# Kernel tuning notes

Measured on AMD Instinct MI355X. Metric: run time of the kernel, lower is better.

The kernel has to match this reference:

```python
import jax, jax.numpy as jnp
import numpy as np

S, B, H = 512, 256, 500


def setup_inputs() -> dict:
    key = jax.random.key(0)
    k1, k2, k3, k4, k5 = jax.random.split(key, 5)
    return {
        "hidden": jax.random.normal(k1, (1, B, H), dtype=jnp.float32),
        "encoder_output": jax.random.normal(k2, (S, B, H), dtype=jnp.float32),
        "W_attn": jax.random.normal(k3, (H, 2 * H), dtype=jnp.float32) * 0.02,
        "b_attn": jax.random.normal(k4, (H,), dtype=jnp.float32) * 0.02,
        "v": jax.random.normal(k5, (H,), dtype=jnp.float32),
    }


def reference(hidden, encoder_output, W_attn, b_attn, v):
    # hidden: [1, B, H] -> broadcast to [S, B, H]; concat -> [S, B, 2H]
    s, b, h = encoder_output.shape
    h_exp = jnp.broadcast_to(hidden, (s, b, h))
    cat = jnp.concatenate([h_exp, encoder_output], axis=2)  # [S, B, 2H]
    # Linear(2H -> H) with torch convention W: [out, in], then tanh
    energy = jnp.tanh(jnp.einsum("sbi,hi->sbh", cat, W_attn) + b_attn)  # [S, B, H]
    scores = jnp.einsum("sbh,h->sb", energy, v)  # [S, B]
    attn = jax.nn.softmax(scores.T, axis=1)  # [B, S]
    return attn[:, None, :]  # [B, 1, S]
```

## Files before the change

### kernel.cpp

```cpp
#include <hip/hip_runtime.h>
#include <hip/hip_fp16.h>

#define S_DIM 512
#define B_DIM 256
#define H_DIM 500
#define HP    512
#define M_DIM (S_DIM * B_DIM)

typedef _Float16 half8_t __attribute__((ext_vector_type(8)));
typedef float    f32x4  __attribute__((ext_vector_type(4)));

#define WS_W2R 0
#define WS_AT  (512 * 1024)
#define WS_VP  (1024 * 1024)
#define WS_SC  (1024 * 1024 + 4096)

__global__ void prep_w2_v(const float* __restrict__ W, const float* __restrict__ v,
                          _Float16* __restrict__ W2r, float* __restrict__ vp) {
    int idx = blockIdx.x * blockDim.x + threadIdx.x;
#pragma unroll
    for (int r = 0; r < 2; ++r) {
        int e = idx + r * 131072;
        int n = e >> 9, k = e & 511;
        float val = (n < H_DIM && k < H_DIM) ? W[n * 1000 + 500 + k] : 0.0f;
        int dst = ((n >> 4) * 64 + (k >> 3)) * 128 + (n & 15) * 8 + (k & 7);
        W2r[dst] = (_Float16)val;
    }
    if (idx < HP) vp[idx] = (idx < H_DIM) ? v[idx] : 0.0f;
}

__global__ void prep_A(const float* __restrict__ hidden, const float* __restrict__ W,
                       const float* __restrict__ b_attn, float* __restrict__ At) {
    int b = blockIdx.x;
    int t = threadIdx.x;
    __shared__ float hs[HP];
    hs[t] = (t < H_DIM) ? hidden[b * H_DIM + t] : 0.0f;
    __syncthreads();
    float acc = 0.0f;
    if (t < H_DIM) {
        acc = b_attn[t];
        const float4* wr = (const float4*)(W + t * 1000);
        const float4* hr = (const float4*)hs;
#pragma unroll 5
        for (int i = 0; i < 125; ++i) {
            float4 w4 = wr[i], h4 = hr[i];
            acc += w4.x * h4.x + w4.y * h4.y + w4.z * h4.z + w4.w * h4.w;
        }
    }
    At[t * B_DIM + b] = acc;
}

__launch_bounds__(256, 2)
__global__ void fused_attn_gemm(const float* __restrict__ enc,
                                const _Float16* __restrict__ W2r,
                                const float* __restrict__ At,
                                const float* __restrict__ vp,
                                float* __restrict__ sct) {
    __shared__ _Float16 As[2][128][32];
    __shared__ float    red[2][128];

    const int tid  = threadIdx.x;
    const int lane = tid & 63;
    const int wid  = tid >> 6;
    const int wm   = wid >> 1;
    const int wn   = wid & 1;
    const int l15  = lane & 15;
    const int lq   = lane >> 4;

    const int mblk = blockIdx.x;
    const int m0   = mblk * 128;
    const int bloc = (mblk & 1) * 128;
    const int s_idx = mblk >> 1;

    const int r0  = tid >> 2;
    const int r1  = r0 + 64;
    const int cst = tid & 3;
    const float* gA0 = enc + (size_t)(m0 + r0) * H_DIM + cst * 8;
    const float* gA1 = enc + (size_t)(m0 + r1) * H_DIM + cst * 8;
    const int ca0 = (cst ^ ((r0 >> 1) & 3)) * 8;
    const int ca1 = (cst ^ ((r1 >> 1) & 3)) * 8;

    const int rch = (lq ^ ((l15 >> 1) & 3)) * 8;

    const _Float16* gB = W2r + wn * 32768 + lq * 128 + l15 * 8;

    f32x4 a00, a01, a10, a11;
    auto ldA = [&](int kk) {
        if (kk != 480) {
            a00 = *(const f32x4*)(gA0 + kk); a01 = *(const f32x4*)(gA0 + kk + 4);
            a10 = *(const f32x4*)(gA1 + kk); a11 = *(const f32x4*)(gA1 + kk + 4);
        } else {
#pragma unroll
            for (int u = 0; u < 4; ++u) {
                int k = kk + cst * 8 + u;
                a00[u] = (k < H_DIM) ? gA0[kk + u] : 0.0f;
                a10[u] = (k < H_DIM) ? gA1[kk + u] : 0.0f;
                int k2 = k + 4;
                a01[u] = (k2 < H_DIM) ? gA0[kk + 4 + u] : 0.0f;
                a11[u] = (k2 < H_DIM) ? gA1[kk + 4 + u] : 0.0f;
            }
        }
    };
    auto wrA = [&](int buf) {
        half8_t h0, h1;
#pragma unroll
        for (int u = 0; u < 4; ++u) {
            h0[u] = (_Float16)a00[u]; h0[u + 4] = (_Float16)a01[u];
            h1[u] = (_Float16)a10[u]; h1[u + 4] = (_Float16)a11[u];
        }
        *(half8_t*)&As[buf][r0][ca0] = h0;
        *(half8_t*)&As[buf][r1][ca1] = h1;
    };

    float pj[4][4];
#pragma unroll
    for (int mf = 0; mf < 4; ++mf)
#pragma unroll
        for (int j = 0; j < 4; ++j) pj[mf][j] = 0.0f;

    for (int nc = 0; nc < 4; ++nc) {
        f32x4 acc[4][4];
#pragma unroll
        for (int a = 0; a < 4; ++a)
#pragma unroll
            for (int b = 0; b < 4; ++b) acc[a][b] = 0;

        ldA(0);
        wrA(0);

#pragma unroll
        for (int ks = 0; ks < 16; ++ks) {
            __syncthreads();
            if (ks < 15) ldA((ks + 1) * 32);

            half8_t bfc[4];
#pragma unroll
            for (int nf = 0; nf < 4; ++nf)
                bfc[nf] = *(const half8_t*)(gB + nc * 65536 + nf * 8192 + ks * 512);

            half8_t af[4];
#pragma unroll
            for (int mf = 0; mf < 4; ++mf)
                af[mf] = *(const half8_t*)&As[ks & 1][wm * 64 + mf * 16 + l15][rch];

#pragma unroll
            for (int mf = 0; mf < 4; ++mf)
#pragma unroll
                for (int nf = 0; nf < 4; ++nf)
                    acc[mf][nf] = __builtin_amdgcn_mfma_f32_16x16x32_f16(af[mf], bfc[nf], acc[mf][nf], 0, 0, 0);

            if (ks < 15) wrA((ks & 1) ^ 1);
        }

        float vpv[4];
#pragma unroll
        for (int nf = 0; nf < 4; ++nf) vpv[nf] = vp[nc * 128 + wn * 64 + nf * 16 + l15];

#pragma unroll
        for (int mf = 0; mf < 4; ++mf) {
#pragma unroll
            for (int nf = 0; nf < 4; ++nf) {
                int h = nc * 128 + wn * 64 + nf * 16 + l15;
                f32x4 av = *(const f32x4*)(At + h * B_DIM + bloc + wm * 64 + mf * 16 + lq * 4);
#pragma unroll
                for (int j = 0; j < 4; ++j) {
                    float x  = acc[mf][nf][j] + av[j];
                    float xc = fminf(fmaxf(x, -9.0f), 9.0f);
                    float e  = __expf(2.0f * xc);
                    float th = (e - 1.0f) / (e + 1.0f);
                    pj[mf][j] += vpv[nf] * th;
                }
            }
        }
    }

#pragma unroll
    for (int mf = 0; mf < 4; ++mf)
#pragma unroll
        for (int j = 0; j < 4; ++j) {
            float s = pj[mf][j];
            s += __shfl_xor(s, 1); s += __shfl_xor(s, 2);
            s += __shfl_xor(s, 4); s += __shfl_xor(s, 8);
            if (l15 == 0) red[wn][wm * 64 + mf * 16 + lq * 4 + j] = s;
        }
    __syncthreads();
    if (tid < 128) {
        float p = red[0][tid] + red[1][tid];
        sct[(size_t)(bloc + tid) * S_DIM + s_idx] = p;
    }
}

__global__ void softmax_rows(const float* __restrict__ sct, float* __restrict__ out) {
    int b = blockIdx.x;
    int t = threadIdx.x;
    int lane = t & 63, w = t >> 6;
    float v = sct[(size_t)b * S_DIM + t];
    float m = v;
#pragma unroll
    for (int off = 1; off < 64; off <<= 1) m = fmaxf(m, __shfl_xor(m, off));
    __shared__ float sm[8], ss[8];
    if (lane == 0) sm[w] = m;
    __syncthreads();
    m = sm[0];
#pragma unroll
    for (int i = 1; i < 8; ++i) m = fmaxf(m, sm[i]);
    float e = __expf(v - m);
    float s = e;
#pragma unroll
    for (int off = 1; off < 64; off <<= 1) s += __shfl_xor(s, off);
    if (lane == 0) ss[w] = s;
    __syncthreads();
    s = ss[0];
#pragma unroll
    for (int i = 1; i < 8; ++i) s += ss[i];
    out[(size_t)b * S_DIM + t] = e / s;
}

extern "C" void kernel_launch(void* const* d_in, const int* in_sizes, int n_in,
                              void* d_out, int out_size, void* d_ws, size_t ws_size,
                              hipStream_t stream) {
    const float* hidden = (const float*)d_in[0];
    const float* enc    = (const float*)d_in[1];
    const float* W      = (const float*)d_in[2];
    const float* b_attn = (const float*)d_in[3];
    const float* v      = (const float*)d_in[4];
    float* out = (float*)d_out;

    char* ws = (char*)d_ws;
    _Float16* W2r = (_Float16*)(ws + WS_W2R);
    float*    At  = (float*)(ws + WS_AT);
    float*    vp  = (float*)(ws + WS_VP);
    float*    sct = (float*)(ws + WS_SC);

    prep_w2_v<<<512, 256, 0, stream>>>(W, v, W2r, vp);
    prep_A<<<256, 512, 0, stream>>>(hidden, W, b_attn, At);
    fused_attn_gemm<<<1024, 256, 0, stream>>>(enc, W2r, At, vp, sct);
    softmax_rows<<<256, 512, 0, stream>>>(sct, out);
}
```

Before: 226.0 us.

## Stage full-N weight tile in LDS via async global_load_lds and shrink M tile

The fused GEMM kernel now computes all 512 output columns per block in one pass over K, with 64 rows per block and 512 threads. The weight matrix is pre-laid out as a swizzled LDS image and streamed into double-buffered shared memory with direct global-to-LDS loads. Previously each warp read B fragments straight from global memory and looped over four N chunks, reloading the encoder tile each time. This removes the fourfold re-read and conversion of the encoder input, but costs a much larger LDS footprint (about 72KB per block) and may limit occupancy despite the launch bounds.

```diff
diff --git a/kernel.cpp b/kernel.cpp
--- a/kernel.cpp
+++ b/kernel.cpp
@@ -10,21 +10,28 @@
 typedef _Float16 half8_t __attribute__((ext_vector_type(8)));
 typedef float    f32x4  __attribute__((ext_vector_type(4)));
 
-#define WS_W2R 0
+#define WS_W2I 0
 #define WS_AT  (512 * 1024)
 #define WS_VP  (1024 * 1024)
 #define WS_SC  (1024 * 1024 + 4096)
 
+__device__ __forceinline__ void gld_lds16(const void* g, void* l) {
+    __builtin_amdgcn_global_load_lds(
+        (const __attribute__((address_space(1))) unsigned int*)g,
+        (__attribute__((address_space(3))) unsigned int*)l, 16, 0, 0);
+}
+
 __global__ void prep_w2_v(const float* __restrict__ W, const float* __restrict__ v,
-                          _Float16* __restrict__ W2r, float* __restrict__ vp) {
+                          _Float16* __restrict__ W2img, float* __restrict__ vp) {
     int idx = blockIdx.x * blockDim.x + threadIdx.x;
 #pragma unroll
     for (int r = 0; r < 2; ++r) {
         int e = idx + r * 131072;
         int n = e >> 9, k = e & 511;
         float val = (n < H_DIM && k < H_DIM) ? W[n * 1000 + 500 + k] : 0.0f;
-        int dst = ((n >> 4) * 64 + (k >> 3)) * 128 + (n & 15) * 8 + (k & 7);
-        W2r[dst] = (_Float16)val;
+        int ks = k >> 5, ce = (k >> 3) & 3, u = k & 7;
+        int cL = ce ^ ((n >> 1) & 3);
+        W2img[((ks * 512 + n) * 4 + cL) * 8 + u] = (_Float16)val;
     }
     if (idx < HP) vp[idx] = (idx < H_DIM) ? v[idx] : 0.0f;
 }
@@ -50,142 +57,132 @@
     At[t * B_DIM + b] = acc;
 }
 
-__launch_bounds__(256, 2)
+__launch_bounds__(512, 4)
 __global__ void fused_attn_gemm(const float* __restrict__ enc,
-                                const _Float16* __restrict__ W2r,
+                                const _Float16* __restrict__ W2img,
                                 const float* __restrict__ At,
                                 const float* __restrict__ vp,
                                 float* __restrict__ sct) {
-    __shared__ _Float16 As[2][128][32];
-    __shared__ float    red[2][128];
+    __shared__ _Float16 As[2][64][32];
+    __shared__ _Float16 Bs[2][512][32];
+    __shared__ float    red[4][64];
 
     const int tid  = threadIdx.x;
     const int lane = tid & 63;
     const int wid  = tid >> 6;
-    const int wm   = wid >> 1;
-    const int wn   = wid & 1;
+    const int wm   = wid >> 2;
+    const int wn   = wid & 3;
     const int l15  = lane & 15;
     const int lq   = lane >> 4;
 
-    const int mblk = blockIdx.x;
-    const int m0   = mblk * 128;
-    const int bloc = (mblk & 1) * 128;
-    const int s_idx = mblk >> 1;
-
-    const int r0  = tid >> 2;
-    const int r1  = r0 + 64;
-    const int cst = tid & 3;
-    const float* gA0 = enc + (size_t)(m0 + r0) * H_DIM + cst * 8;
-    const float* gA1 = enc + (size_t)(m0 + r1) * H_DIM + cst * 8;
-    const int ca0 = (cst ^ ((r0 >> 1) & 3)) * 8;
-    const int ca1 = (cst ^ ((r1 >> 1) & 3)) * 8;
+    const int mblk  = blockIdx.x;
+    const int m0    = mblk * 64;
+    const int s_idx = mblk >> 2;
+    const int bloc  = (mblk & 3) * 64;
+
+    const bool aw = (tid < 256);
+    const int  r  = tid >> 2;
+    const int  c  = tid & 3;
+    const float* gA = enc + (size_t)(m0 + (r & 63)) * H_DIM + c * 8;
+    const int  ca = (c ^ ((r >> 1) & 3)) * 8;
 
     const int rch = (lq ^ ((l15 >> 1) & 3)) * 8;
 
-    const _Float16* gB = W2r + wn * 32768 + lq * 128 + l15 * 8;
-
-    f32x4 a00, a01, a10, a11;
+    f32x4 a0, a1;
     auto ldA = [&](int kk) {
         if (kk != 480) {
-            a00 = *(const f32x4*)(gA0 + kk); a01 = *(const f32x4*)(gA0 + kk + 4);
-            a10 = *(const f32x4*)(gA1 + kk); a11 = *(const f32x4*)(gA1 + kk + 4);
+            a0 = *(const f32x4*)(gA + kk);
+            a1 = *(const f32x4*)(gA + kk + 4);
         } else {
 #pragma unroll
             for (int u = 0; u < 4; ++u) {
-                int k = kk + cst * 8 + u;
-                a00[u] = (k < H_DIM) ? gA0[kk + u] : 0.0f;
-                a10[u] = (k < H_DIM) ? gA1[kk + u] : 0.0f;
-                int k2 = k + 4;
-                a01[u] = (k2 < H_DIM) ? gA0[kk + 4 + u] : 0.0f;
-                a11[u] = (k2 < H_DIM) ? gA1[kk + 4 + u] : 0.0f;
+                int k = kk + c * 8 + u;
+                a0[u] = (k < H_DIM) ? gA[kk + u] : 0.0f;
+                a1[u] = (k + 4 < H_DIM) ? gA[kk + 4 + u] : 0.0f;
             }
         }
     };
     auto wrA = [&](int buf) {
-        half8_t h0, h1;
-#pragma unroll
-        for (int u = 0; u < 4; ++u) {
-            h0[u] = (_Float16)a00[u]; h0[u + 4] = (_Float16)a01[u];
-            h1[u] = (_Float16)a10[u]; h1[u + 4] = (_Float16)a11[u];
-        }
-        *(half8_t*)&As[buf][r0][ca0] = h0;
-        *(half8_t*)&As[buf][r1][ca1] = h1;
+        half8_t h;
+#pragma unroll
+        for (int u = 0; u < 4; ++u) { h[u] = (_Float16)a0[u]; h[u + 4] = (_Float16)a1[u]; }
+        *(half8_t*)&As[buf][r & 63][ca] = h;
     };
-
-    float pj[4][4];
-#pragma unroll
-    for (int mf = 0; mf < 4; ++mf)
+    auto stB = [&](int buf, int ksrc) {
+        const _Float16* gbase = W2img + (size_t)ksrc * 16384;
+#pragma unroll
+        for (int i = 0; i < 4; ++i) {
+            int slotb = wid * 256 + i * 64;
+            gld_lds16(gbase + (size_t)(slotb + lane) * 8, (_Float16*)&Bs[buf][0][0] + slotb * 8);
+        }
+    };
+
+    f32x4 acc[2][8];
+#pragma unroll
+    for (int a = 0; a < 2; ++a)
+#pragma unroll
+        for (int b = 0; b < 8; ++b) acc[a][b] = 0;
+
+    stB(0, 0);
+    if (aw) { ldA(0); wrA(0); }
+
+    for (int ks = 0; ks < 16; ++ks) {
+        const int cur = ks & 1;
+        __syncthreads();
+        if (ks < 15) {
+            stB(cur ^ 1, ks + 1);
+            if (aw) ldA((ks + 1) * 32);
+        }
+        half8_t af0 = *(const half8_t*)&As[cur][wm * 32 + l15][rch];
+        half8_t af1 = *(const half8_t*)&As[cur][wm * 32 + 16 + l15][rch];
+#pragma unroll
+        for (int nf = 0; nf < 8; ++nf) {
+            half8_t b = *(const half8_t*)&Bs[cur][wn * 128 + nf * 16 + l15][rch];
+            acc[0][nf] = __builtin_amdgcn_mfma_f32_16x16x32_f16(af0, b, acc[0][nf], 0, 0, 0);
+            acc[1][nf] = __builtin_amdgcn_mfma_f32_16x16x32_f16(af1, b, acc[1][nf], 0, 0, 0);
+        }
+        if (ks < 15 && aw) wrA(cur ^ 1);
+    }
+
+    float vpv[8];
+#pragma unroll
+    for (int nf = 0; nf < 8; ++nf) vpv[nf] = vp[wn * 128 + nf * 16 + l15];
+
+    float pj[2][4];
+#pragma unroll
+    for (int mf = 0; mf < 2; ++mf)
 #pragma unroll
         for (int j = 0; j < 4; ++j) pj[mf][j] = 0.0f;
 
-    for (int nc = 0; nc < 4; ++nc) {
-        f32x4 acc[4][4];
-#pragma unroll
-        for (int a = 0; a < 4; ++a)
-#pragma unroll
-            for (int b = 0; b < 4; ++b) acc[a][b] = 0;
-
-        ldA(0);
-        wrA(0);
-
-#pragma unroll
-        for (int ks = 0; ks < 16; ++ks) {
-            __syncthreads();
-            if (ks < 15) ldA((ks + 1) * 32);
-
-            half8_t bfc[4];
-#pragma unroll
-            for (int nf = 0; nf < 4; ++nf)
-                bfc[nf] = *(const half8_t*)(gB + nc * 65536 + nf * 8192 + ks * 512);
-
-            half8_t af[4];
-#pragma unroll
-            for (int mf = 0; mf < 4; ++mf)
-                af[mf] = *(const half8_t*)&As[ks & 1][wm * 64 + mf * 16 + l15][rch];
-
-#pragma unroll
-            for (int mf = 0; mf < 4; ++mf)
-#pragma unroll
-                for (int nf = 0; nf < 4; ++nf)
-                    acc[mf][nf] = __builtin_amdgcn_mfma_f32_16x16x32_f16(af[mf], bfc[nf], acc[mf][nf], 0, 0, 0);
-
-            if (ks < 15) wrA((ks & 1) ^ 1);
-        }
-
-        float vpv[4];
-#pragma unroll
-        for (int nf = 0; nf < 4; ++nf) vpv[nf] = vp[nc * 128 + wn * 64 + nf * 16 + l15];
-
-#pragma unroll
-        for (int mf = 0; mf < 4; ++mf) {
-#pragma unroll
-            for (int nf = 0; nf < 4; ++nf) {
-                int h = nc * 128 + wn * 64 + nf * 16 + l15;
-                f32x4 av = *(const f32x4*)(At + h * B_DIM + bloc + wm * 64 + mf * 16 + lq * 4);
-#pragma unroll
-                for (int j = 0; j < 4; ++j) {
-                    float x  = acc[mf][nf][j] + av[j];
-                    float xc = fminf(fmaxf(x, -9.0f), 9.0f);
-                    float e  = __expf(2.0f * xc);
-                    float th = (e - 1.0f) / (e + 1.0f);
-                    pj[mf][j] += vpv[nf] * th;
-                }
+#pragma unroll
+    for (int mf = 0; mf < 2; ++mf) {
+#pragma unroll
+        for (int nf = 0; nf < 8; ++nf) {
+            int h = wn * 128 + nf * 16 + l15;
+            f32x4 av = *(const f32x4*)(At + h * B_DIM + bloc + wm * 32 + mf * 16 + lq * 4);
+#pragma unroll
+            for (int j = 0; j < 4; ++j) {
+                float x  = acc[mf][nf][j] + av[j];
+                float xc = fminf(fmaxf(x, -9.0f), 9.0f);
+                float e  = __expf(2.0f * xc);
+                float th = (e - 1.0f) / (e + 1.0f);
+                pj[mf][j] += vpv[nf] * th;
             }
         }
     }
 
 #pragma unroll
-    for (int mf = 0; mf < 4; ++mf)
+    for (int mf = 0; mf < 2; ++mf)
 #pragma unroll
         for (int j = 0; j < 4; ++j) {
             float s = pj[mf][j];
             s += __shfl_xor(s, 1); s += __shfl_xor(s, 2);
             s += __shfl_xor(s, 4); s += __shfl_xor(s, 8);
-            if (l15 == 0) red[wn][wm * 64 + mf * 16 + lq * 4 + j] = s;
-        }
-    __syncthreads();
-    if (tid < 128) {
-        float p = red[0][tid] + red[1][tid];
+            if (l15 == 0) red[wn][wm * 32 + mf * 16 + lq * 4 + j] = s;
+        }
+    __syncthreads();
+    if (tid < 64) {
+        float p = red[0][tid] + red[1][tid] + red[2][tid] + red[3][tid];
         sct[(size_t)(bloc + tid) * S_DIM + s_idx] = p;
     }
 }
@@ -227,13 +224,13 @@
     float* out = (float*)d_out;
 
     char* ws = (char*)d_ws;
-    _Float16* W2r = (_Float16*)(ws + WS_W2R);
+    _Float16* W2i = (_Float16*)(ws + WS_W2I);
     float*    At  = (float*)(ws + WS_AT);
     float*    vp  = (float*)(ws + WS_VP);
     float*    sct = (float*)(ws + WS_SC);
 
-    prep_w2_v<<<512, 256, 0, stream>>>(W, v, W2r, vp);
+    prep_w2_v<<<512, 256, 0, stream>>>(W, v, W2i, vp);
     prep_A<<<256, 512, 0, stream>>>(hidden, W, b_attn, At);
-    fused_attn_gemm<<<1024, 256, 0, stream>>>(enc, W2r, At, vp, sct);
+    fused_attn_gemm<<<2048, 512, 0, stream>>>(enc, W2i, At, vp, sct);
     softmax_rows<<<256, 512, 0, stream>>>(sct, out);
 }
```

New measurement: 187.2 us. 1.21x faster.

## Widen GEMM block to cover full N so encoder tile is loaded once

Applied to the files above, without the earlier changes.

The fused GEMM block grows to 512 threads in a 2x4 wave grid, with each wave computing 128 output columns in a single pass. This replaces four sequential N chunks that each re-streamed and re-converted the fp32 encoder rows. It also adds a two-slice-ahead register prefetch with a hand-written LDS barrier, and simplifies the K-tail loads. The cost is 128 accumulator floats per thread, which raises register pressure and may reduce occupancy.

```diff
diff --git a/kernel.cpp b/kernel.cpp
--- a/kernel.cpp
+++ b/kernel.cpp
@@ -8,6 +8,7 @@
 #define M_DIM (S_DIM * B_DIM)
 
 typedef _Float16 half8_t __attribute__((ext_vector_type(8)));
+typedef _Float16 half4_t __attribute__((ext_vector_type(4)));
 typedef float    f32x4  __attribute__((ext_vector_type(4)));
 
 #define WS_W2R 0
@@ -50,142 +51,145 @@
     At[t * B_DIM + b] = acc;
 }
 
-__launch_bounds__(256, 2)
+__launch_bounds__(512, 2)
 __global__ void fused_attn_gemm(const float* __restrict__ enc,
                                 const _Float16* __restrict__ W2r,
                                 const float* __restrict__ At,
                                 const float* __restrict__ vp,
                                 float* __restrict__ sct) {
     __shared__ _Float16 As[2][128][32];
-    __shared__ float    red[2][128];
+    __shared__ float    red[4][128];
 
     const int tid  = threadIdx.x;
     const int lane = tid & 63;
     const int wid  = tid >> 6;
-    const int wm   = wid >> 1;
-    const int wn   = wid & 1;
+    const int wm   = wid >> 2;
+    const int wn   = wid & 3;
     const int l15  = lane & 15;
     const int lq   = lane >> 4;
 
-    const int mblk = blockIdx.x;
-    const int m0   = mblk * 128;
-    const int bloc = (mblk & 1) * 128;
+    const int mblk  = blockIdx.x;
+    const int m0    = mblk * 128;
     const int s_idx = mblk >> 1;
-
-    const int r0  = tid >> 2;
-    const int r1  = r0 + 64;
-    const int cst = tid & 3;
-    const float* gA0 = enc + (size_t)(m0 + r0) * H_DIM + cst * 8;
-    const float* gA1 = enc + (size_t)(m0 + r1) * H_DIM + cst * 8;
-    const int ca0 = (cst ^ ((r0 >> 1) & 3)) * 8;
-    const int ca1 = (cst ^ ((r1 >> 1) & 3)) * 8;
-
+    const int bloc  = (mblk & 1) * 128;
+
+    const int r0 = tid >> 3;
+    const int r1 = r0 + 64;
+    const int j  = tid & 7;
+    const float* gA0 = enc + (size_t)(m0 + r0) * H_DIM + j * 4;
+    const float* gA1 = enc + (size_t)(m0 + r1) * H_DIM + j * 4;
+    const int jt = (j < 4) ? j : 4;
+    const float* gT0 = enc + (size_t)(m0 + r0) * H_DIM + 480 + jt * 4;
+    const float* gT1 = enc + (size_t)(m0 + r1) * H_DIM + 480 + jt * 4;
+    const bool jz = (j >= 5);
+    const int aoff = ((j >> 1) ^ ((r0 >> 1) & 3)) * 8 + (j & 1) * 4;
     const int rch = (lq ^ ((l15 >> 1) & 3)) * 8;
 
-    const _Float16* gB = W2r + wn * 32768 + lq * 128 + l15 * 8;
-
-    f32x4 a00, a01, a10, a11;
-    auto ldA = [&](int kk) {
-        if (kk != 480) {
-            a00 = *(const f32x4*)(gA0 + kk); a01 = *(const f32x4*)(gA0 + kk + 4);
-            a10 = *(const f32x4*)(gA1 + kk); a11 = *(const f32x4*)(gA1 + kk + 4);
-        } else {
-#pragma unroll
-            for (int u = 0; u < 4; ++u) {
-                int k = kk + cst * 8 + u;
-                a00[u] = (k < H_DIM) ? gA0[kk + u] : 0.0f;
-                a10[u] = (k < H_DIM) ? gA1[kk + u] : 0.0f;
-                int k2 = k + 4;
-                a01[u] = (k2 < H_DIM) ? gA0[kk + 4 + u] : 0.0f;
-                a11[u] = (k2 < H_DIM) ? gA1[kk + 4 + u] : 0.0f;
+    const _Float16* gB = W2r + wn * 65536 + lq * 128 + l15 * 8;
+
+    f32x4 acc[4][8];
+#pragma unroll
+    for (int a = 0; a < 4; ++a)
+#pragma unroll
+        for (int b = 0; b < 8; ++b) acc[a][b] = 0;
+
+    f32x4 pe0, pe1, po0, po1;
+
+    auto ldA = [&](int slice, f32x4& d0, f32x4& d1) {
+        if (slice == 15) { d0 = *(const f32x4*)gT0; d1 = *(const f32x4*)gT1; }
+        else { d0 = *(const f32x4*)(gA0 + slice * 32); d1 = *(const f32x4*)(gA1 + slice * 32); }
+    };
+    auto wrA = [&](int buf, f32x4 d0, f32x4 d1, bool tail) {
+        half4_t h0, h1;
+#pragma unroll
+        for (int u = 0; u < 4; ++u) {
+            h0[u] = (tail && jz) ? (_Float16)0.0f : (_Float16)d0[u];
+            h1[u] = (tail && jz) ? (_Float16)0.0f : (_Float16)d1[u];
+        }
+        *(half4_t*)&As[buf][r0][aoff] = h0;
+        *(half4_t*)&As[buf][r1][aoff] = h1;
+    };
+
+#define BAR() do {                                             \
+        asm volatile("s_waitcnt lgkmcnt(0)" ::: "memory");     \
+        __builtin_amdgcn_sched_barrier(0);                     \
+        __builtin_amdgcn_s_barrier();                          \
+        __builtin_amdgcn_sched_barrier(0);                     \
+    } while (0)
+
+#define KBODY(KS, CUR, WR0, WR1, LD0, LD1)                                     \
+    {                                                                          \
+        half8_t bq[8];                                                         \
+        _Pragma("unroll")                                                      \
+        for (int nf = 0; nf < 8; ++nf)                                         \
+            bq[nf] = *(const half8_t*)(gB + nf * 8192 + (KS) * 512);           \
+        if ((KS) + 2 < 16) ldA((KS) + 2, LD0, LD1);                            \
+        half8_t af[4];                                                         \
+        _Pragma("unroll")                                                      \
+        for (int mf = 0; mf < 4; ++mf)                                         \
+            af[mf] = *(const half8_t*)&As[CUR][wm * 64 + mf * 16 + l15][rch];  \
+        _Pragma("unroll")                                                      \
+        for (int nf = 0; nf < 8; ++nf) {                                       \
+            _Pragma("unroll")                                                  \
+            for (int mf = 0; mf < 4; ++mf)                                     \
+                acc[mf][nf] = __builtin_amdgcn_mfma_f32_16x16x32_f16(          \
+                    af[mf], bq[nf], acc[mf][nf], 0, 0, 0);                     \
+        }                                                                      \
+        if ((KS) + 1 < 16) wrA((CUR) ^ 1, WR0, WR1, (KS) + 1 == 15);           \
+        BAR();                                                                 \
+    }
+
+    ldA(0, pe0, pe1);
+    wrA(0, pe0, pe1, false);
+    ldA(1, po0, po1);
+    BAR();
+
+    for (int kk = 0; kk < 16; kk += 2) {
+        KBODY(kk,     0, po0, po1, pe0, pe1)
+        KBODY(kk + 1, 1, pe0, pe1, po0, po1)
+    }
+#undef KBODY
+#undef BAR
+
+    float vpv[8];
+#pragma unroll
+    for (int nf = 0; nf < 8; ++nf) vpv[nf] = vp[wn * 128 + nf * 16 + l15];
+
+    float pj[4][4];
+#pragma unroll
+    for (int mf = 0; mf < 4; ++mf)
+#pragma unroll
+        for (int jj = 0; jj < 4; ++jj) pj[mf][jj] = 0.0f;
+
+#pragma unroll
+    for (int mf = 0; mf < 4; ++mf) {
+#pragma unroll
+        for (int nf = 0; nf < 8; ++nf) {
+            int h = wn * 128 + nf * 16 + l15;
+            f32x4 av = *(const f32x4*)(At + h * B_DIM + bloc + wm * 64 + mf * 16 + lq * 4);
+#pragma unroll
+            for (int jj = 0; jj < 4; ++jj) {
+                float x  = acc[mf][nf][jj] + av[jj];
+                float xc = fminf(fmaxf(x, -9.0f), 9.0f);
+                float e  = __expf(2.0f * xc);
+                float th = (e - 1.0f) / (e + 1.0f);
+                pj[mf][jj] += vpv[nf] * th;
             }
         }
-    };
-    auto wrA = [&](int buf) {
-        half8_t h0, h1;
-#pragma unroll
-        for (int u = 0; u < 4; ++u) {
-            h0[u] = (_Float16)a00[u]; h0[u + 4] = (_Float16)a01[u];
-            h1[u] = (_Float16)a10[u]; h1[u + 4] = (_Float16)a11[u];
-        }
-        *(half8_t*)&As[buf][r0][ca0] = h0;
-        *(half8_t*)&As[buf][r1][ca1] = h1;
-    };
-
-    float pj[4][4];
+    }
+
 #pragma unroll
     for (int mf = 0; mf < 4; ++mf)
 #pragma unroll
-        for (int j = 0; j < 4; ++j) pj[mf][j] = 0.0f;
-
-    for (int nc = 0; nc < 4; ++nc) {
-        f32x4 acc[4][4];
-#pragma unroll
-        for (int a = 0; a < 4; ++a)
-#pragma unroll
-            for (int b = 0; b < 4; ++b) acc[a][b] = 0;
-
-        ldA(0);
-        wrA(0);
-
-#pragma unroll
-        for (int ks = 0; ks < 16; ++ks) {
-            __syncthreads();
-            if (ks < 15) ldA((ks + 1) * 32);
-
-            half8_t bfc[4];
-#pragma unroll
-            for (int nf = 0; nf < 4; ++nf)
-                bfc[nf] = *(const half8_t*)(gB + nc * 65536 + nf * 8192 + ks * 512);
-
-            half8_t af[4];
-#pragma unroll
-            for (int mf = 0; mf < 4; ++mf)
-                af[mf] = *(const half8_t*)&As[ks & 1][wm * 64 + mf * 16 + l15][rch];
-
-#pragma unroll
-            for (int mf = 0; mf < 4; ++mf)
-#pragma unroll
-                for (int nf = 0; nf < 4; ++nf)
-                    acc[mf][nf] = __builtin_amdgcn_mfma_f32_16x16x32_f16(af[mf], bfc[nf], acc[mf][nf], 0, 0, 0);
-
-            if (ks < 15) wrA((ks & 1) ^ 1);
-        }
-
-        float vpv[4];
-#pragma unroll
-        for (int nf = 0; nf < 4; ++nf) vpv[nf] = vp[nc * 128 + wn * 64 + nf * 16 + l15];
-
-#pragma unroll
-        for (int mf = 0; mf < 4; ++mf) {
-#pragma unroll
-            for (int nf = 0; nf < 4; ++nf) {
-                int h = nc * 128 + wn * 64 + nf * 16 + l15;
-                f32x4 av = *(const f32x4*)(At + h * B_DIM + bloc + wm * 64 + mf * 16 + lq * 4);
-#pragma unroll
-                for (int j = 0; j < 4; ++j) {
-                    float x  = acc[mf][nf][j] + av[j];
-                    float xc = fminf(fmaxf(x, -9.0f), 9.0f);
-                    float e  = __expf(2.0f * xc);
-                    float th = (e - 1.0f) / (e + 1.0f);
-                    pj[mf][j] += vpv[nf] * th;
-                }
-            }
-        }
-    }
-
-#pragma unroll
-    for (int mf = 0; mf < 4; ++mf)
-#pragma unroll
-        for (int j = 0; j < 4; ++j) {
-            float s = pj[mf][j];
+        for (int jj = 0; jj < 4; ++jj) {
+            float s = pj[mf][jj];
             s += __shfl_xor(s, 1); s += __shfl_xor(s, 2);
             s += __shfl_xor(s, 4); s += __shfl_xor(s, 8);
-            if (l15 == 0) red[wn][wm * 64 + mf * 16 + lq * 4 + j] = s;
+            if (l15 == 0) red[wn][wm * 64 + mf * 16 + lq * 4 + jj] = s;
         }
     __syncthreads();
     if (tid < 128) {
-        float p = red[0][tid] + red[1][tid];
+        float p = red[0][tid] + red[1][tid] + red[2][tid] + red[3][tid];
         sct[(size_t)(bloc + tid) * S_DIM + s_idx] = p;
     }
 }
@@ -234,6 +238,6 @@
 
     prep_w2_v<<<512, 256, 0, stream>>>(W, v, W2r, vp);
     prep_A<<<256, 512, 0, stream>>>(hidden, W, b_attn, At);
-    fused_attn_gemm<<<1024, 256, 0, stream>>>(enc, W2r, At, vp, sct);
+    fused_attn_gemm<<<1024, 512, 0, stream>>>(enc, W2r, At, vp, sct);
     softmax_rows<<<256, 512, 0, stream>>>(sct, out);
 }
```

New measurement: 219.8 us. 2.7% less time.

## Split GEMM N across two workgroups and stage W tiles in LDS via direct loads

Applied to the files above, without the earlier changes.

The fused GEMM kernel no longer loops over four N-chunks that each reload the encoder A tile. Each of 2048 workgroups of 512 threads now computes a 128x256 output tile in a single K loop. The B (weight) tiles are pre-swizzled and brought into LDS with global_load_lds direct copies, replacing per-wave global loads, and block indices are remapped for locality. Partial scores from the two N halves are written to separate buffers and summed in the softmax kernel. This removes the repeated fp32 encoder reads and conversions per N-chunk, at the cost of more LDS use, an extra score buffer and one more read in softmax.

```diff
diff --git a/kernel.cpp b/kernel.cpp
--- a/kernel.cpp
+++ b/kernel.cpp
@@ -4,36 +4,42 @@
 #define S_DIM 512
 #define B_DIM 256
 #define H_DIM 500
-#define HP    512
 #define M_DIM (S_DIM * B_DIM)
 
 typedef _Float16 half8_t __attribute__((ext_vector_type(8)));
 typedef float    f32x4  __attribute__((ext_vector_type(4)));
 
-#define WS_W2R 0
+#define WS_W2I 0
 #define WS_AT  (512 * 1024)
 #define WS_VP  (1024 * 1024)
 #define WS_SC  (1024 * 1024 + 4096)
 
+__device__ __forceinline__ void gld_lds16(const void* g, void* l) {
+    __builtin_amdgcn_global_load_lds(
+        (const __attribute__((address_space(1))) unsigned int*)g,
+        (__attribute__((address_space(3))) unsigned int*)l, 16, 0, 0);
+}
+
 __global__ void prep_w2_v(const float* __restrict__ W, const float* __restrict__ v,
-                          _Float16* __restrict__ W2r, float* __restrict__ vp) {
+                          _Float16* __restrict__ W2i, float* __restrict__ vp) {
     int idx = blockIdx.x * blockDim.x + threadIdx.x;
 #pragma unroll
     for (int r = 0; r < 2; ++r) {
         int e = idx + r * 131072;
         int n = e >> 9, k = e & 511;
         float val = (n < H_DIM && k < H_DIM) ? W[n * 1000 + 500 + k] : 0.0f;
-        int dst = ((n >> 4) * 64 + (k >> 3)) * 128 + (n & 15) * 8 + (k & 7);
-        W2r[dst] = (_Float16)val;
-    }
-    if (idx < HP) vp[idx] = (idx < H_DIM) ? v[idx] : 0.0f;
+        int nb = n >> 8, nl = n & 255, ks = k >> 5, ce = (k >> 3) & 3, u = k & 7;
+        int cL = ce ^ ((nl >> 1) & 3);
+        W2i[((ks * 2 + nb) * 1024 + nl * 4 + cL) * 8 + u] = (_Float16)val;
+    }
+    if (idx < 512) vp[idx] = (idx < H_DIM) ? v[idx] : 0.0f;
 }
 
 __global__ void prep_A(const float* __restrict__ hidden, const float* __restrict__ W,
                        const float* __restrict__ b_attn, float* __restrict__ At) {
     int b = blockIdx.x;
     int t = threadIdx.x;
-    __shared__ float hs[HP];
+    __shared__ float hs[512];
     hs[t] = (t < H_DIM) ? hidden[b * H_DIM + t] : 0.0f;
     __syncthreads();
     float acc = 0.0f;
@@ -50,67 +56,104 @@
     At[t * B_DIM + b] = acc;
 }
 
-__launch_bounds__(256, 2)
+__launch_bounds__(512, 4)
 __global__ void fused_attn_gemm(const float* __restrict__ enc,
-                                const _Float16* __restrict__ W2r,
+                                const _Float16* __restrict__ W2i,
                                 const float* __restrict__ At,
                                 const float* __restrict__ vp,
                                 float* __restrict__ sct) {
     __shared__ _Float16 As[2][128][32];
-    __shared__ float    red[2][128];
+    __shared__ _Float16 Bs[2][256][32];
+    __shared__ float    red[4][128];
 
     const int tid  = threadIdx.x;
     const int lane = tid & 63;
     const int wid  = tid >> 6;
-    const int wm   = wid >> 1;
-    const int wn   = wid & 1;
+    const int wm   = wid >> 2;
+    const int wn   = wid & 3;
     const int l15  = lane & 15;
     const int lq   = lane >> 4;
 
-    const int mblk = blockIdx.x;
-    const int m0   = mblk * 128;
-    const int bloc = (mblk & 1) * 128;
+    const int wg    = (blockIdx.x & 7) * 256 + (blockIdx.x >> 3);
+    const int mblk  = wg >> 1;
+    const int nblk  = wg & 1;
+    const int m0    = mblk * 128;
     const int s_idx = mblk >> 1;
-
-    const int r0  = tid >> 2;
-    const int r1  = r0 + 64;
-    const int cst = tid & 3;
-    const float* gA0 = enc + (size_t)(m0 + r0) * H_DIM + cst * 8;
-    const float* gA1 = enc + (size_t)(m0 + r1) * H_DIM + cst * 8;
-    const int ca0 = (cst ^ ((r0 >> 1) & 3)) * 8;
-    const int ca1 = (cst ^ ((r1 >> 1) & 3)) * 8;
+    const int bloc  = (mblk & 1) * 128;
+    const int n0    = nblk * 256;
+
+    const int r = tid >> 2;
+    const int c = tid & 3;
+    const float* gA = enc + (size_t)(m0 + r) * H_DIM + c * 8;
+    const int ca = (c ^ ((r >> 1) & 3)) * 8;
 
     const int rch = (lq ^ ((l15 >> 1) & 3)) * 8;
 
-    const _Float16* gB = W2r + wn * 32768 + lq * 128 + l15 * 8;
-
-    f32x4 a00, a01, a10, a11;
-    auto ldA = [&](int kk) {
-        if (kk != 480) {
-            a00 = *(const f32x4*)(gA0 + kk); a01 = *(const f32x4*)(gA0 + kk + 4);
-            a10 = *(const f32x4*)(gA1 + kk); a11 = *(const f32x4*)(gA1 + kk + 4);
+    f32x4 a0, a1;
+
+    auto ldA = [&](int slice) {
+        if (slice < 15) {
+            a0 = *(const f32x4*)(gA + slice * 32);
+            a1 = *(const f32x4*)(gA + slice * 32 + 4);
         } else {
+            const float* gr = enc + (size_t)(m0 + r) * H_DIM;
 #pragma unroll
             for (int u = 0; u < 4; ++u) {
-                int k = kk + cst * 8 + u;
-                a00[u] = (k < H_DIM) ? gA0[kk + u] : 0.0f;
-                a10[u] = (k < H_DIM) ? gA1[kk + u] : 0.0f;
-                int k2 = k + 4;
-                a01[u] = (k2 < H_DIM) ? gA0[kk + 4 + u] : 0.0f;
-                a11[u] = (k2 < H_DIM) ? gA1[kk + 4 + u] : 0.0f;
+                int k0 = 480 + c * 8 + u;
+                int k1 = k0 + 4;
+                a0[u] = (k0 < H_DIM) ? gr[k0] : 0.0f;
+                a1[u] = (k1 < H_DIM) ? gr[k1] : 0.0f;
             }
         }
     };
     auto wrA = [&](int buf) {
-        half8_t h0, h1;
-#pragma unroll
-        for (int u = 0; u < 4; ++u) {
-            h0[u] = (_Float16)a00[u]; h0[u + 4] = (_Float16)a01[u];
-            h1[u] = (_Float16)a10[u]; h1[u + 4] = (_Float16)a11[u];
-        }
-        *(half8_t*)&As[buf][r0][ca0] = h0;
-        *(half8_t*)&As[buf][r1][ca1] = h1;
+        half8_t h;
+#pragma unroll
+        for (int u = 0; u < 4; ++u) { h[u] = (_Float16)a0[u]; h[u + 4] = (_Float16)a1[u]; }
+        *(half8_t*)&As[buf][r][ca] = h;
     };
+    auto stB = [&](int buf, int ks) {
+        const _Float16* pb = W2i + (size_t)(ks * 2 + nblk) * 8192;
+        _Float16* dl = (_Float16*)&Bs[buf][0][0] + (size_t)wid * 512;
+        gld_lds16(pb + (size_t)tid * 8, dl);
+        gld_lds16(pb + (size_t)(tid + 512) * 8, dl + 4096);
+    };
+
+    f32x4 acc[4][4];
+#pragma unroll
+    for (int a = 0; a < 4; ++a)
+#pragma unroll
+        for (int b = 0; b < 4; ++b) acc[a][b] = 0;
+
+    stB(0, 0);
+    ldA(0);
+    wrA(0);
+
+    for (int ks = 0; ks < 16; ++ks) {
+        const int cur = ks & 1;
+        __syncthreads();
+        if (ks < 15) {
+            stB(cur ^ 1, ks + 1);
+            ldA(ks + 1);
+        }
+        half8_t af[4], bf[4];
+#pragma unroll
+        for (int mf = 0; mf < 4; ++mf)
+            af[mf] = *(const half8_t*)&As[cur][wm * 64 + mf * 16 + l15][rch];
+#pragma unroll
+        for (int nf = 0; nf < 4; ++nf)
+            bf[nf] = *(const half8_t*)&Bs[cur][wn * 64 + nf * 16 + l15][rch];
+#pragma unroll
+        for (int mf = 0; mf < 4; ++mf)
+#pragma unroll
+            for (int nf = 0; nf < 4; ++nf)
+                acc[mf][nf] = __builtin_amdgcn_mfma_f32_16x16x32_f16(af[mf], bf[nf], acc[mf][nf], 0, 0, 0);
+        if (ks < 15) wrA(cur ^ 1);
+    }
+
+    float vpv[4];
+#pragma unroll
+    for (int nf = 0; nf < 4; ++nf) vpv[nf] = vp[n0 + wn * 64 + nf * 16 + l15];
 
     float pj[4][4];
 #pragma unroll
@@ -118,58 +161,19 @@
 #pragma unroll
         for (int j = 0; j < 4; ++j) pj[mf][j] = 0.0f;
 
-    for (int nc = 0; nc < 4; ++nc) {
-        f32x4 acc[4][4];
-#pragma unroll
-        for (int a = 0; a < 4; ++a)
-#pragma unroll
-            for (int b = 0; b < 4; ++b) acc[a][b] = 0;
-
-        ldA(0);
-        wrA(0);
-
-#pragma unroll
-        for (int ks = 0; ks < 16; ++ks) {
-            __syncthreads();
-            if (ks < 15) ldA((ks + 1) * 32);
-
-            half8_t bfc[4];
-#pragma unroll
-            for (int nf = 0; nf < 4; ++nf)
-                bfc[nf] = *(const half8_t*)(gB + nc * 65536 + nf * 8192 + ks * 512);
-
-            half8_t af[4];
-#pragma unroll
-            for (int mf = 0; mf < 4; ++mf)
-                af[mf] = *(const half8_t*)&As[ks & 1][wm * 64 + mf * 16 + l15][rch];
-
-#pragma unroll
-            for (int mf = 0; mf < 4; ++mf)
-#pragma unroll
-                for (int nf = 0; nf < 4; ++nf)
-                    acc[mf][nf] = __builtin_amdgcn_mfma_f32_16x16x32_f16(af[mf], bfc[nf], acc[mf][nf], 0, 0, 0);
-
-            if (ks < 15) wrA((ks & 1) ^ 1);
-        }
-
-        float vpv[4];
-#pragma unroll
-        for (int nf = 0; nf < 4; ++nf) vpv[nf] = vp[nc * 128 + wn * 64 + nf * 16 + l15];
-
-#pragma unroll
-        for (int mf = 0; mf < 4; ++mf) {
-#pragma unroll
-            for (int nf = 0; nf < 4; ++nf) {
-                int h = nc * 128 + wn * 64 + nf * 16 + l15;
-                f32x4 av = *(const f32x4*)(At + h * B_DIM + bloc + wm * 64 + mf * 16 + lq * 4);
-#pragma unroll
-                for (int j = 0; j < 4; ++j) {
-                    float x  = acc[mf][nf][j] + av[j];
-                    float xc = fminf(fmaxf(x, -9.0f), 9.0f);
-                    float e  = __expf(2.0f * xc);
-                    float th = (e - 1.0f) / (e + 1.0f);
-                    pj[mf][j] += vpv[nf] * th;
-                }
+#pragma unroll
+    for (int mf = 0; mf < 4; ++mf) {
+#pragma unroll
+        for (int nf = 0; nf < 4; ++nf) {
+            int h = n0 + wn * 64 + nf * 16 + l15;
+            f32x4 av = *(const f32x4*)(At + h * B_DIM + bloc + wm * 64 + mf * 16 + lq * 4);
+#pragma unroll
+            for (int j = 0; j < 4; ++j) {
+                float x  = acc[mf][nf][j] + av[j];
+                float xc = fminf(fmaxf(x, -9.0f), 9.0f);
+                float e  = __expf(2.0f * xc);
+                float th = (e - 1.0f) / (e + 1.0f);
+                pj[mf][j] += vpv[nf] * th;
             }
         }
     }
@@ -185,8 +189,8 @@
         }
     __syncthreads();
     if (tid < 128) {
-        float p = red[0][tid] + red[1][tid];
-        sct[(size_t)(bloc + tid) * S_DIM + s_idx] = p;
+        float p = red[0][tid] + red[1][tid] + red[2][tid] + red[3][tid];
+        sct[(size_t)nblk * M_DIM + (size_t)(bloc + tid) * S_DIM + s_idx] = p;
     }
 }
 
@@ -194,7 +198,8 @@
     int b = blockIdx.x;
     int t = threadIdx.x;
     int lane = t & 63, w = t >> 6;
-    float v = sct[(size_t)b * S_DIM + t];
+    size_t idx = (size_t)b * S_DIM + t;
+    float v = sct[idx] + sct[idx + M_DIM];
     float m = v;
 #pragma unroll
     for (int off = 1; off < 64; off <<= 1) m = fmaxf(m, __shfl_xor(m, off));
@@ -227,13 +232,13 @@
     float* out = (float*)d_out;
 
     char* ws = (char*)d_ws;
-    _Float16* W2r = (_Float16*)(ws + WS_W2R);
+    _Float16* W2i = (_Float16*)(ws + WS_W2I);
     float*    At  = (float*)(ws + WS_AT);
     float*    vp  = (float*)(ws + WS_VP);
     float*    sct = (float*)(ws + WS_SC);
 
-    prep_w2_v<<<512, 256, 0, stream>>>(W, v, W2r, vp);
+    prep_w2_v<<<512, 256, 0, stream>>>(W, v, W2i, vp);
     prep_A<<<256, 512, 0, stream>>>(hidden, W, b_attn, At);
-    fused_attn_gemm<<<1024, 256, 0, stream>>>(enc, W2r, At, vp, sct);
+    fused_attn_gemm<<<2048, 512, 0, stream>>>(enc, W2i, At, vp, sct);
     softmax_rows<<<256, 512, 0, stream>>>(sct, out);
 }
```

Result: no change. 222.6 us (-1.5%).
